# Performance work log

Measured on AMD Instinct MI355X. Metric: run time of the kernel, lower is better.

The kernel has to match this reference:

```python
import jax, jax.numpy as jnp
import numpy as np
from functools import partial

B, S, D, L, O, V = 32, 1024, 256, 4, 64, 5  # batch, seq, d_model, n_layers, output_dim, vocab
EPS = 1e-5
RC_MAP = jnp.array([3, 2, 1, 0, 4], dtype=jnp.int32)  # A<->T, C<->G, N->N


def layernorm(x, g, b):
    m = jnp.mean(x, axis=-1, keepdims=True)
    v = jnp.mean((x - m) ** 2, axis=-1, keepdims=True)
    return (x - m) * jax.lax.rsqrt(v + EPS) * g + b


def gru(x, w_ih, w_hh, b_ih, b_hh):
    """torch nn.GRU (single layer, batch_first) equivalent.
    x: (B,S,D); w_ih: (3H,D); w_hh: (3H,H); gates ordered r,z,n."""
    H = w_hh.shape[1]
    # precompute input contributions for all timesteps: (S,B,3H)
    xi = (jnp.einsum('bsd,gd->bsg', x, w_ih) + b_ih).transpose(1, 0, 2)

    def step(h, xt):
        gh = h @ w_hh.T + b_hh                      # (B,3H)
        xr, xz, xn = jnp.split(xt, 3, axis=-1)
        hr, hz, hn = jnp.split(gh, 3, axis=-1)
        r = jax.nn.sigmoid(xr + hr)
        z = jax.nn.sigmoid(xz + hz)
        n = jnp.tanh(xn + r * hn)
        h2 = (1.0 - z) * n + z * h
        return h2, h2

    h0 = jnp.zeros((x.shape[0], H), dtype=x.dtype)
    _, out = jax.lax.scan(step, h0, xi)
    return out.transpose(1, 0, 2)                   # (B,S,H)


def setup_inputs() -> dict:
    key = jax.random.key(0)
    ks = jax.random.split(key, 32)
    n = lambda k, shp, s=0.02: (jax.random.normal(k, shp, dtype=jnp.float32) * s)
    inp = {
        'tokens': jax.random.randint(ks[0], (B, S), 0, V),
        'emb':    n(ks[1], (V, D), 1.0),
        'pos':    n(ks[2], (1, S, D)),
        # per-layer stacked params (leading dim L)
        'ln_g':   jnp.ones((L, D), jnp.float32),
        'ln_b':   jnp.zeros((L, D), jnp.float32),
        'wih_f':  n(ks[3], (L, 3 * D, D)),
        'whh_f':  n(ks[4], (L, 3 * D, D)),
        'bih_f':  n(ks[5], (L, 3 * D)),
        'bhh_f':  n(ks[6], (L, 3 * D)),
        'wih_r':  n(ks[7], (L, 3 * D, D)),
        'whh_r':  n(ks[8], (L, 3 * D, D)),
        'bih_r':  n(ks[9], (L, 3 * D)),
        'bhh_r':  n(ks[10], (L, 3 * D)),
        'wg':     n(ks[11], (L, D, 2 * D)),
        'bg':     n(ks[12], (L, D)),
        'wo':     n(ks[13], (L, D, D)),
        'bo':     n(ks[14], (L, D)),
        'fn_g':   jnp.ones((D,), jnp.float32),
        'fn_b':   jnp.zeros((D,), jnp.float32),
        'pw':     n(ks[15], (O, D)),
        'pb':     n(ks[16], (O,)),
        'pln_g':  jnp.ones((O,), jnp.float32),
        'pln_b':  jnp.zeros((O,), jnp.float32),
    }
    return inp


def reference(tokens, emb, pos, ln_g, ln_b,
              wih_f, whh_f, bih_f, bhh_f,
              wih_r, whh_r, bih_r, bhh_r,
              wg, bg, wo, bo, fn_g, fn_b, pw, pb, pln_g, pln_b):
    def encode(tok):
        h = emb[tok] + pos[:, :tok.shape[1], :]      # (B,S,D)
        for i in range(L):
            hn = layernorm(h, ln_g[i], ln_b[i])
            f = gru(hn, wih_f[i], whh_f[i], bih_f[i], bhh_f[i])
            r = jnp.flip(gru(jnp.flip(hn, 1), wih_r[i], whh_r[i], bih_r[i], bhh_r[i]), 1)
            g = jax.nn.sigmoid(jnp.concatenate([f, r], -1) @ wg[i].T + bg[i])
            c = g * f + (1.0 - g) * r
            h = c @ wo[i].T + bo[i] + h              # residual
        return layernorm(h, fn_g, fn_b)

    h = encode(tokens)
    rc_tokens = jnp.flip(RC_MAP[tokens], -1)         # reverse-complement
    h_rc = encode(rc_tokens)
    pooled = (h.mean(1) + h_rc.mean(1)) * 0.5        # (B,D)
    p = layernorm(pooled @ pw.T + pb, pln_g, pln_b)
    return jax.nn.gelu(p, approximate=False)         # (B,O)
```

## Files before the change

kernel.cpp:

```cpp
#include <hip/hip_runtime.h>
#include <stdint.h>

#define DEV __device__ __forceinline__

typedef unsigned short u16;
typedef __attribute__((ext_vector_type(8))) __bf16 bf16x8;
typedef __attribute__((ext_vector_type(4))) float f32x4;

DEV float bf2f(u16 u) {
    unsigned v = ((unsigned)u) << 16;
    float f;
    __builtin_memcpy(&f, &v, 4);
    return f;
}
DEV u16 f2bf(float x) {
    unsigned u;
    __builtin_memcpy(&u, &x, 4);
    return (u16)((u + 0x7FFFu + ((u >> 16) & 1u)) >> 16);
}
DEV float sigf(float x) {
    float e = __builtin_amdgcn_exp2f(-1.442695040888963f * x);
    return __builtin_amdgcn_rcpf(1.0f + e);
}
DEV f32x4 mfma16(bf16x8 a, bf16x8 b, f32x4 c) {
    return __builtin_amdgcn_mfma_f32_16x16x32_bf16(a, b, c, 0, 0, 0);
}

static constexpr size_t XROW = 1536;
static constexpr size_t XE = 32768 * XROW;
static constexpr float NL2E = -1.442695040888963f;
static constexpr float P2L2E = 2.885390081777927f;

__global__ void convert_w(const float* __restrict__ src, u16* __restrict__ dst,
                          int n_per, int stride_l, int total) {
    int idx = blockIdx.x * 256 + threadIdx.x;
    if (idx >= total) return;
    int l = idx / n_per;
    int r = idx - l * n_per;
    dst[(size_t)l * stride_l + r] = f2bf(src[idx]);
}

__global__ void convert_whh(const float* __restrict__ src, u16* __restrict__ dst, int dir_ofs) {
    int idx = blockIdx.x * 256 + threadIdx.x;
    int l = idx / 196608;
    int r = idx - l * 196608;
    float S = ((r >> 16) < 2) ? NL2E : P2L2E;
    dst[(size_t)l * 393216 + dir_ofs + r] = f2bf(src[idx] * S);
}

__global__ void convert_wih(const float* __restrict__ src, const float* __restrict__ lng,
                            u16* __restrict__ dst, int dir_ofs) {
    int idx = blockIdx.x * 256 + threadIdx.x;
    int l = idx / 196608;
    int r = idx - l * 196608;
    int k = idx & 255;
    float S = ((r >> 16) < 2) ? NL2E : P2L2E;
    dst[(size_t)l * 393216 + dir_ofs + r] = f2bf(src[idx] * lng[l * 256 + k] * S);
}

__global__ void head_vecs_kernel(const float* __restrict__ wihf, const float* __restrict__ wihr,
                                 const float* __restrict__ bihf, const float* __restrict__ bihr,
                                 const float* __restrict__ bhhf, const float* __restrict__ bhhr,
                                 const float* __restrict__ lng, const float* __restrict__ lnb,
                                 float* __restrict__ env, float* __restrict__ cvec) {
    int w = threadIdx.x >> 6, lane = threadIdx.x & 63;
    int row = blockIdx.x * 4 + w;
    int l = row / 1536;
    int n1536 = row - l * 1536;
    int dir = n1536 >= 768;
    int n = n1536 - dir * 768;
    const float* W = (dir ? wihr : wihf) + ((size_t)l * 768 + n) * 256 + lane * 4;
    float4 wv = *(const float4*)W;
    float4 gv = *(const float4*)(lng + l * 256 + lane * 4);
    float4 bv = *(const float4*)(lnb + l * 256 + lane * 4);
    float es = wv.x * gv.x + wv.y * gv.y + wv.z * gv.z + wv.w * gv.w;
    float cs = wv.x * bv.x + wv.y * bv.y + wv.z * bv.z + wv.w * bv.w;
#pragma unroll
    for (int off = 1; off < 64; off <<= 1) {
        es += __shfl_xor(es, off);
        cs += __shfl_xor(cs, off);
    }
    if (lane == 0) {
        float S = (n < 512) ? NL2E : P2L2E;
        float c = cs + (dir ? bihr : bihf)[l * 768 + n];
        if (n < 512) c += (dir ? bhhr : bhhf)[l * 768 + n];
        env[row] = es * S;
        cvec[row] = c * S;
    }
}

__global__ void embed_kernel(const int* __restrict__ tok, const float* __restrict__ emb,
                             const float* __restrict__ pos, u16* __restrict__ h) {
    int row = blockIdx.x;
    int k = threadIdx.x;
    int e = row >> 15;
    int rem = row & 32767;
    int b = rem >> 10;
    int s = rem & 1023;
    int t0 = (e == 0) ? tok[b * 1024 + s] : tok[b * 1024 + (1023 - s)];
    if (e == 1) t0 = (t0 < 4) ? (3 - t0) : 4;
    h[(size_t)row * 256 + k] = f2bf(emb[t0 * 256 + k] + pos[s * 256 + k]);
}

__global__ void ln_stats_kernel(const u16* __restrict__ h, float2* __restrict__ stats) {
    int w = threadIdx.x >> 6, lane = threadIdx.x & 63;
    int row = blockIdx.x * 4 + w;
    int e = row >> 15;
    int rem = row & 32767;
    int b = rem >> 10;
    int s = rem & 1023;
    ushort4 v = *(const ushort4*)(h + (size_t)row * 256 + lane * 4);
    float x0 = bf2f(v.x), x1 = bf2f(v.y), x2 = bf2f(v.z), x3 = bf2f(v.w);
    float sum = x0 + x1 + x2 + x3;
    float sq = x0 * x0 + x1 * x1 + x2 * x2 + x3 * x3;
#pragma unroll
    for (int off = 1; off < 64; off <<= 1) {
        sum += __shfl_xor(sum, off);
        sq += __shfl_xor(sq, off);
    }
    if (lane == 0) {
        float mean = sum * (1.0f / 256.0f);
        float var = sq * (1.0f / 256.0f) - mean * mean;
        stats[e * 32768 + s * 32 + b] = make_float2(mean, rsqrtf(var + 1e-5f));
    }
}

template <int OP>
__global__ __launch_bounds__(256, 2) void gemm_bt(
    const u16* __restrict__ hin, const u16* __restrict__ Bw,
    const float* __restrict__ bias0, const float* __restrict__ bias1,
    u16* xibuf, const float2* __restrict__ stats, u16* hres) {
    constexpr int KK = (OP == 1) ? 512 : 256;
    constexpr int NKB = KK / 64;
    __shared__ __align__(16) u16 As[2][128 * 64];
    __shared__ __align__(16) u16 Bs[2][128 * 64];
    const int tid = threadIdx.x;
    const int lane = tid & 63, w = tid >> 6;
    const int l15 = lane & 15, q = lane >> 4;
    const int l8 = lane & 7, r8 = lane >> 3;
    const int e = blockIdx.z;
    const int m0 = blockIdx.x * 128, n0 = blockIdx.y * 128;
    const int wm = w & 1, wn = w >> 1;

    uint4 ra[4], rb[4];
    auto loadS = [&](int kb) {
#pragma unroll
        for (int i = 0; i < 4; ++i) {
            int row = w * 32 + i * 8 + r8;
            int c = l8 ^ (row & 7);
            int mrow = m0 + row;
            const u16* ap;
            if constexpr (OP == 0) {
                int bb = mrow & 31, ss = mrow >> 5;
                ap = hin + ((size_t)e * 32768 + bb * 1024 + ss) * 256 + kb * 64;
            } else if constexpr (OP == 1) {
                int colbase = (kb >= 4) ? 768 : 0;
                ap = xibuf + (size_t)e * XE + (size_t)mrow * XROW + colbase + (kb & 3) * 64;
            } else {
                ap = xibuf + (size_t)e * XE + (size_t)mrow * XROW + 256 + kb * 64;
            }
            ra[i] = *(const uint4*)(ap + c * 8);
            rb[i] = *(const uint4*)(Bw + (size_t)(n0 + row) * KK + kb * 64 + c * 8);
        }
    };
    auto writeS = [&](int buf) {
#pragma unroll
        for (int i = 0; i < 4; ++i) {
            int row = w * 32 + i * 8 + r8;
            *(uint4*)&As[buf][row * 64 + l8 * 8] = ra[i];
            *(uint4*)&Bs[buf][row * 64 + l8 * 8] = rb[i];
        }
    };

    f32x4 acc[4][4];
#pragma unroll
    for (int i = 0; i < 4; ++i)
#pragma unroll
        for (int j = 0; j < 4; ++j) acc[i][j] = (f32x4){0.f, 0.f, 0.f, 0.f};

    loadS(0);
    writeS(0);
    for (int kb = 0; kb < NKB; ++kb) {
        if (kb + 1 < NKB) loadS(kb + 1);
        __syncthreads();
        const int buf = kb & 1;
#pragma unroll
        for (int kt = 0; kt < 2; ++kt) {
            bf16x8 af[4], bfr[4];
#pragma unroll
            for (int i = 0; i < 4; ++i) {
                int rowa = wm * 64 + i * 16 + l15;
                int rowb = wn * 64 + i * 16 + l15;
                int c = kt * 4 + q;
                af[i] = *(const bf16x8*)&As[buf][rowa * 64 + (c ^ (rowa & 7)) * 8];
                bfr[i] = *(const bf16x8*)&Bs[buf][rowb * 64 + (c ^ (rowb & 7)) * 8];
            }
#pragma unroll
            for (int i = 0; i < 4; ++i)
#pragma unroll
                for (int j = 0; j < 4; ++j) acc[i][j] = mfma16(af[i], bfr[j], acc[i][j]);
        }
        if (kb + 1 < NKB) writeS((kb + 1) & 1);
    }

#pragma unroll
    for (int i = 0; i < 4; ++i) {
        const int mb = m0 + wm * 64 + i * 16 + q * 4;
        float2 st[4];
        if constexpr (OP == 0) {
#pragma unroll
            for (int r = 0; r < 4; ++r) st[r] = stats[e * 32768 + mb + r];
        }
#pragma unroll
        for (int jt = 0; jt < 4; ++jt) {
            const int nn = n0 + wn * 64 + jt * 16 + l15;
            f32x4 a = acc[i][jt];
            if constexpr (OP == 0) {
                const float en = bias0[nn], cn = bias1[nn];
#pragma unroll
                for (int r = 0; r < 4; ++r) {
                    float val = a[r] * st[r].y - st[r].x * st[r].y * en + cn;
                    xibuf[(size_t)e * XE + (size_t)(mb + r) * XROW + nn] = f2bf(val);
                }
            } else if constexpr (OP == 1) {
                const float bs = bias0[nn];
#pragma unroll
                for (int r = 0; r < 4; ++r) {
                    u16* xr_ = xibuf + (size_t)e * XE + (size_t)(mb + r) * XROW;
                    float gg = sigf(a[r] + bs);
                    float fv = bf2f(xr_[nn]), rv = bf2f(xr_[768 + nn]);
                    xr_[256 + nn] = f2bf(gg * fv + (1.0f - gg) * rv);
                }
            } else {
                const float bs = bias0[nn];
#pragma unroll
                for (int r = 0; r < 4; ++r) {
                    const int mm = mb + r;
                    size_t idx = ((size_t)e * 32768 + (size_t)(mm & 31) * 1024 + (mm >> 5)) * 256 + nn;
                    hres[idx] = f2bf(bf2f(hres[idx]) + a[r] + bs);
                }
            }
        }
    }
}

__global__ __launch_bounds__(512, 2) void scan_kernel(
    u16* xi, const u16* __restrict__ whh,
    const float* __restrict__ bhhf, const float* __restrict__ bhhr) {
    __shared__ __align__(16) u16 h_lds[16 * 264];
    const int tid = threadIdx.x;
    const int w = tid >> 6, lane = tid & 63;
    const int l15 = lane & 15, q = lane >> 4;
    const int bid = blockIdx.x;
    const int bh = bid & 1, d = (bid >> 1) & 1, e = bid >> 2;
    const int jb = w * 32;

    const u16* W = whh + (size_t)d * 196608;
    bf16x8 wf[3][2][8];
#pragma unroll
    for (int g = 0; g < 3; ++g)
#pragma unroll
        for (int jc = 0; jc < 2; ++jc)
#pragma unroll
            for (int kt = 0; kt < 8; ++kt)
                wf[g][jc][kt] = *(const bf16x8*)(
                    W + (size_t)(g * 256 + jb + jc * 16 + l15) * 256 + kt * 32 + q * 8);

    const float* bnp = (d ? bhhr : bhhf) + 512;
    f32x4 bn[2];
#pragma unroll
    for (int jc = 0; jc < 2; ++jc)
#pragma unroll
        for (int r = 0; r < 4; ++r) bn[jc][r] = P2L2E * bnp[jb + jc * 16 + q * 4 + r];

    const int s0 = d ? 1023 : 0;
    const ptrdiff_t step = (d ? -32 : 32) * (ptrdiff_t)XROW;
    u16* p = xi + (size_t)e * XE + (size_t)(s0 * 32 + bh * 16 + l15) * XROW + d * 768 + jb + q * 4;

    const int lrow = l15 * 264;
    const int jcol = jb + q * 4;

    ushort4 xvv[3][2];
#pragma unroll
    for (int g = 0; g < 3; ++g)
#pragma unroll
        for (int jc = 0; jc < 2; ++jc)
            xvv[g][jc] = *(const ushort4*)(p + g * 256 + jc * 16);

    for (int t = 0; t < 1024; ++t) {
        f32x4 a0[2], a1[2], a2[2];
#pragma unroll
        for (int jc = 0; jc < 2; ++jc) {
            a0[jc] = (f32x4){0.f, 0.f, 0.f, 0.f};
            a1[jc] = (f32x4){0.f, 0.f, 0.f, 0.f};
            a2[jc] = bn[jc];
        }
        if (t > 0) {
#pragma unroll
            for (int kt = 0; kt < 8; ++kt) {
                bf16x8 hb = *(const bf16x8*)&h_lds[lrow + kt * 32 + q * 8];
#pragma unroll
                for (int jc = 0; jc < 2; ++jc) {
                    a0[jc] = mfma16(wf[0][jc][kt], hb, a0[jc]);
                    a1[jc] = mfma16(wf[1][jc][kt], hb, a1[jc]);
                    a2[jc] = mfma16(wf[2][jc][kt], hb, a2[jc]);
                }
            }
        }
        ushort4 hs[2];
#pragma unroll
        for (int jc = 0; jc < 2; ++jc) {
            ushort4 hp4 = (t > 0) ? *(const ushort4*)&h_lds[lrow + jcol + jc * 16]
                                  : (ushort4){0, 0, 0, 0};
            u16 hr[4];
#pragma unroll
            for (int r = 0; r < 4; ++r) {
                float xr = bf2f(((const u16*)&xvv[0][jc])[r]);
                float xz = bf2f(((const u16*)&xvv[1][jc])[r]);
                float xn = bf2f(((const u16*)&xvv[2][jc])[r]);
                float rg = __builtin_amdgcn_rcpf(1.0f + __builtin_amdgcn_exp2f(xr + a0[jc][r]));
                float zg = __builtin_amdgcn_rcpf(1.0f + __builtin_amdgcn_exp2f(xz + a1[jc][r]));
                float E = __builtin_amdgcn_exp2f(__builtin_fmaf(rg, a2[jc][r], xn));
                float ng = (E - 1.0f) * __builtin_amdgcn_rcpf(E + 1.0f);
                float hp = (t > 0) ? bf2f(((const u16*)&hp4)[r]) : 0.f;
                float h2 = __builtin_fmaf(zg, hp - ng, ng);
                hr[r] = f2bf(h2);
            }
            hs[jc] = (ushort4){hr[0], hr[1], hr[2], hr[3]};
        }
        *(ushort4*)(p + 0) = hs[0];
        *(ushort4*)(p + 16) = hs[1];
        __syncthreads();
        *(ushort4*)&h_lds[lrow + jcol] = hs[0];
        *(ushort4*)&h_lds[lrow + jcol + 16] = hs[1];
        __syncthreads();
        if (t + 1 < 1024) {
            p += step;
#pragma unroll
            for (int g = 0; g < 3; ++g)
#pragma unroll
                for (int jc = 0; jc < 2; ++jc)
                    xvv[g][jc] = *(const ushort4*)(p + g * 256 + jc * 16);
        }
    }
}

__global__ __launch_bounds__(256) void pool_head_kernel(
    const u16* __restrict__ h, const float* __restrict__ fng, const float* __restrict__ fnb,
    const float* __restrict__ pw, const float* __restrict__ pb,
    const float* __restrict__ plng, const float* __restrict__ plnb, float* __restrict__ out) {
    __shared__ float pacc[4][256];
    __shared__ float pooled[256];
    const int b = blockIdx.x;
    const int tid = threadIdx.x;
    const int w = tid >> 6, lane = tid & 63;
    float a0 = 0.f, a1 = 0.f, a2 = 0.f, a3 = 0.f;
    for (int rr = w; rr < 2048; rr += 4) {
        int e = rr >> 10, s = rr & 1023;
        const u16* src = h + ((size_t)e * 32768 + (size_t)b * 1024 + s) * 256 + lane * 4;
        ushort4 v = *(const ushort4*)src;
        float x0 = bf2f(v.x), x1 = bf2f(v.y), x2 = bf2f(v.z), x3 = bf2f(v.w);
        float sum = x0 + x1 + x2 + x3;
        float sq = x0 * x0 + x1 * x1 + x2 * x2 + x3 * x3;
#pragma unroll
        for (int off = 1; off < 64; off <<= 1) {
            sum += __shfl_xor(sum, off);
            sq += __shfl_xor(sq, off);
        }
        float mean = sum * (1.0f / 256.0f);
        float var = sq * (1.0f / 256.0f) - mean * mean;
        float rs = rsqrtf(var + 1e-5f);
        a0 += (x0 - mean) * rs;
        a1 += (x1 - mean) * rs;
        a2 += (x2 - mean) * rs;
        a3 += (x3 - mean) * rs;
    }
    pacc[w][lane * 4 + 0] = a0;
    pacc[w][lane * 4 + 1] = a1;
    pacc[w][lane * 4 + 2] = a2;
    pacc[w][lane * 4 + 3] = a3;
    __syncthreads();
    {
        int k = tid;
        float t = pacc[0][k] + pacc[1][k] + pacc[2][k] + pacc[3][k];
        pooled[k] = (t * fng[k] + 2048.0f * fnb[k]) * (0.5f / 1024.0f);
    }
    __syncthreads();
    if (tid < 64) {
        float p = pb[tid];
        const float* wrow = pw + tid * 256;
        for (int k = 0; k < 256; ++k) p += pooled[k] * wrow[k];
        float sum = p;
#pragma unroll
        for (int off = 1; off < 64; off <<= 1) sum += __shfl_xor(sum, off);
        float mean = sum * (1.0f / 64.0f);
        float dv = p - mean;
        float sq = dv * dv;
#pragma unroll
        for (int off = 1; off < 64; off <<= 1) sq += __shfl_xor(sq, off);
        float var = sq * (1.0f / 64.0f);
        float y = dv * rsqrtf(var + 1e-5f) * plng[tid] + plnb[tid];
        out[b * 64 + tid] = y * 0.5f * (1.0f + erff(y * 0.70710678118654752f));
    }
}

extern "C" void kernel_launch(void* const* d_in, const int* in_sizes, int n_in,
                              void* d_out, int out_size, void* d_ws, size_t ws_size,
                              hipStream_t stream) {
    (void)in_sizes; (void)n_in; (void)out_size; (void)ws_size;
    const int* tokens = (const int*)d_in[0];
    const float* emb = (const float*)d_in[1];
    const float* pos = (const float*)d_in[2];
    const float* ln_g = (const float*)d_in[3];
    const float* ln_b = (const float*)d_in[4];
    const float* wih_f = (const float*)d_in[5];
    const float* whh_f = (const float*)d_in[6];
    const float* bih_f = (const float*)d_in[7];
    const float* bhh_f = (const float*)d_in[8];
    const float* wih_r = (const float*)d_in[9];
    const float* whh_r = (const float*)d_in[10];
    const float* bih_r = (const float*)d_in[11];
    const float* bhh_r = (const float*)d_in[12];
    const float* wg = (const float*)d_in[13];
    const float* bg = (const float*)d_in[14];
    const float* wo = (const float*)d_in[15];
    const float* bo = (const float*)d_in[16];
    const float* fn_g = (const float*)d_in[17];
    const float* fn_b = (const float*)d_in[18];
    const float* pw = (const float*)d_in[19];
    const float* pb = (const float*)d_in[20];
    const float* pln_g = (const float*)d_in[21];
    const float* pln_b = (const float*)d_in[22];
    float* out = (float*)d_out;
    char* ws = (char*)d_ws;

    u16* h = (u16*)(ws + 0);
    u16* xi = (u16*)(ws + 33554432);
    u16* wih_cat = (u16*)(ws + 234881024);
    u16* whh_bf = (u16*)(ws + 238026752);
    u16* wg_bf = (u16*)(ws + 241172480);
    u16* wo_bf = (u16*)(ws + 242221056);
    float* env = (float*)(ws + 242745344);
    float* cvec = (float*)(ws + 242769920);
    float2* stats = (float2*)(ws + 242794496);

    convert_wih<<<3072, 256, 0, stream>>>(wih_f, ln_g, wih_cat, 0);
    convert_wih<<<3072, 256, 0, stream>>>(wih_r, ln_g, wih_cat, 196608);
    convert_whh<<<3072, 256, 0, stream>>>(whh_f, whh_bf, 0);
    convert_whh<<<3072, 256, 0, stream>>>(whh_r, whh_bf, 196608);
    convert_w<<<2048, 256, 0, stream>>>(wg, wg_bf, 131072, 131072, 524288);
    convert_w<<<1024, 256, 0, stream>>>(wo, wo_bf, 65536, 65536, 262144);
    head_vecs_kernel<<<1536, 256, 0, stream>>>(wih_f, wih_r, bih_f, bih_r, bhh_f, bhh_r,
                                               ln_g, ln_b, env, cvec);
    embed_kernel<<<65536, 256, 0, stream>>>(tokens, emb, pos, h);

    for (int i = 0; i < 4; ++i) {
        ln_stats_kernel<<<16384, 256, 0, stream>>>(h, stats);
        gemm_bt<0><<<dim3(256, 12, 2), 256, 0, stream>>>(
            h, wih_cat + (size_t)i * 393216, env + i * 1536, cvec + i * 1536,
            xi, stats, nullptr);
        scan_kernel<<<8, 512, 0, stream>>>(
            xi, whh_bf + (size_t)i * 393216, bhh_f + i * 768, bhh_r + i * 768);
        gemm_bt<1><<<dim3(256, 2, 2), 256, 0, stream>>>(
            nullptr, wg_bf + (size_t)i * 131072, bg + i * 256, nullptr,
            xi, nullptr, nullptr);
        gemm_bt<2><<<dim3(256, 2, 2), 256, 0, stream>>>(
            nullptr, wo_bf + (size_t)i * 65536, bo + i * 256, nullptr,
            xi, nullptr, h);
    }
    pool_head_kernel<<<32, 256, 0, stream>>>(h, fn_g, fn_b, pw, pb, pln_g, pln_b, out);
}
```

Before: 10.37 ms.

## Fuse LayerNorm stats into input-projection GEMM with resident A tile

Removes the separate ln_stats kernel and computes per-row mean and rstd inside a new gemm_xi kernel while loading the full 128x256 activation tile into LDS. Each block keeps its A tile resident and loops over all 12 N tiles of the 1536-wide weight, register-prefetching the next B tile. This cuts a kernel launch, the stats round trip through global memory, and the repeated A reloads across N-tile blocks. The cost is a 128KB LDS footprint at one block per CU and only 512 blocks, so there is less parallelism and latency hiding.

```diff
diff --git a/kernel.cpp b/kernel.cpp
--- a/kernel.cpp
+++ b/kernel.cpp
@@ -102,34 +102,146 @@
     h[(size_t)row * 256 + k] = f2bf(emb[t0 * 256 + k] + pos[s * 256 + k]);
 }
 
-__global__ void ln_stats_kernel(const u16* __restrict__ h, float2* __restrict__ stats) {
-    int w = threadIdx.x >> 6, lane = threadIdx.x & 63;
-    int row = blockIdx.x * 4 + w;
-    int e = row >> 15;
-    int rem = row & 32767;
-    int b = rem >> 10;
-    int s = rem & 1023;
-    ushort4 v = *(const ushort4*)(h + (size_t)row * 256 + lane * 4);
-    float x0 = bf2f(v.x), x1 = bf2f(v.y), x2 = bf2f(v.z), x3 = bf2f(v.w);
-    float sum = x0 + x1 + x2 + x3;
-    float sq = x0 * x0 + x1 * x1 + x2 * x2 + x3 * x3;
-#pragma unroll
-    for (int off = 1; off < 64; off <<= 1) {
-        sum += __shfl_xor(sum, off);
-        sq += __shfl_xor(sq, off);
-    }
-    if (lane == 0) {
-        float mean = sum * (1.0f / 256.0f);
-        float var = sq * (1.0f / 256.0f) - mean * mean;
-        stats[e * 32768 + s * 32 + b] = make_float2(mean, rsqrtf(var + 1e-5f));
+__global__ __launch_bounds__(256, 1) void gemm_xi(
+    const u16* __restrict__ hin, const u16* __restrict__ Bw,
+    const float* __restrict__ env, const float* __restrict__ cvec,
+    u16* __restrict__ xibuf) {
+    __shared__ __align__(16) u16 Ah[128 * 256];
+    __shared__ __align__(16) u16 Bsh[128 * 256];
+    __shared__ float2 stats_s[128];
+    const int tid = threadIdx.x;
+    const int lane = tid & 63, w = tid >> 6;
+    const int l15 = lane & 15, q = lane >> 4;
+    const int l8 = lane & 7, r8 = lane >> 3;
+    const int e = blockIdx.z;
+    const int m0 = blockIdx.x * 128;
+    const int wm = w & 1, wn = w >> 1;
+
+    float sm0 = 0.f, sm1 = 0.f, sm2 = 0.f, sm3 = 0.f;
+    float sq0 = 0.f, sq1 = 0.f, sq2 = 0.f, sq3 = 0.f;
+#pragma unroll
+    for (int i = 0; i < 4; ++i) {
+        const int row = w * 32 + i * 8 + r8;
+        const int mrow = m0 + row;
+        const int bb = mrow & 31, ss = mrow >> 5;
+        const u16* ap = hin + ((size_t)e * 32768 + bb * 1024 + ss) * 256;
+        const int c = l8 ^ (row & 7);
+        float s = 0.f, s2 = 0.f;
+#pragma unroll
+        for (int kb = 0; kb < 4; ++kb) {
+            uint4 v = *(const uint4*)(ap + kb * 64 + c * 8);
+            *(uint4*)&Ah[row * 256 + kb * 64 + l8 * 8] = v;
+            const u16* pv = (const u16*)&v;
+#pragma unroll
+            for (int x = 0; x < 8; ++x) {
+                float f = bf2f(pv[x]);
+                s += f;
+                s2 += f * f;
+            }
+        }
+        if (i == 0) { sm0 = s; sq0 = s2; }
+        if (i == 1) { sm1 = s; sq1 = s2; }
+        if (i == 2) { sm2 = s; sq2 = s2; }
+        if (i == 3) { sm3 = s; sq3 = s2; }
+    }
+#pragma unroll
+    for (int off = 1; off < 8; off <<= 1) {
+        sm0 += __shfl_xor(sm0, off); sq0 += __shfl_xor(sq0, off);
+        sm1 += __shfl_xor(sm1, off); sq1 += __shfl_xor(sq1, off);
+        sm2 += __shfl_xor(sm2, off); sq2 += __shfl_xor(sq2, off);
+        sm3 += __shfl_xor(sm3, off); sq3 += __shfl_xor(sq3, off);
+    }
+    if (l8 == 0) {
+#pragma unroll
+        for (int i = 0; i < 4; ++i) {
+            float s = (i == 0) ? sm0 : (i == 1) ? sm1 : (i == 2) ? sm2 : sm3;
+            float s2 = (i == 0) ? sq0 : (i == 1) ? sq1 : (i == 2) ? sq2 : sq3;
+            float mean = s * (1.0f / 256.0f);
+            float var = s2 * (1.0f / 256.0f) - mean * mean;
+            stats_s[w * 32 + i * 8 + r8] = make_float2(mean, rsqrtf(var + 1e-5f));
+        }
+    }
+
+    uint4 rbv[16];
+    auto loadB = [&](int nt) {
+#pragma unroll
+        for (int i = 0; i < 4; ++i) {
+            const int row = w * 32 + i * 8 + r8;
+            const int c = l8 ^ (row & 7);
+            const u16* bp = Bw + (size_t)(nt * 128 + row) * 256;
+#pragma unroll
+            for (int kb = 0; kb < 4; ++kb)
+                rbv[kb * 4 + i] = *(const uint4*)(bp + kb * 64 + c * 8);
+        }
+    };
+    auto writeB = [&]() {
+#pragma unroll
+        for (int i = 0; i < 4; ++i) {
+            const int row = w * 32 + i * 8 + r8;
+#pragma unroll
+            for (int kb = 0; kb < 4; ++kb)
+                *(uint4*)&Bsh[row * 256 + kb * 64 + l8 * 8] = rbv[kb * 4 + i];
+        }
+    };
+    loadB(0);
+    writeB();
+    __syncthreads();
+
+    for (int nt = 0; nt < 12; ++nt) {
+        if (nt + 1 < 12) loadB(nt + 1);
+        f32x4 acc[4][4];
+#pragma unroll
+        for (int i = 0; i < 4; ++i)
+#pragma unroll
+            for (int j = 0; j < 4; ++j) acc[i][j] = (f32x4){0.f, 0.f, 0.f, 0.f};
+#pragma unroll
+        for (int ks = 0; ks < 8; ++ks) {
+            const int K8 = ks * 4 + q;
+            const int kb = K8 >> 3, c = K8 & 7;
+            bf16x8 af[4], bfr[4];
+#pragma unroll
+            for (int i = 0; i < 4; ++i) {
+                int rowa = wm * 64 + i * 16 + l15;
+                int rowb = wn * 64 + i * 16 + l15;
+                af[i] = *(const bf16x8*)&Ah[rowa * 256 + kb * 64 + ((c ^ (rowa & 7)) * 8)];
+                bfr[i] = *(const bf16x8*)&Bsh[rowb * 256 + kb * 64 + ((c ^ (rowb & 7)) * 8)];
+            }
+#pragma unroll
+            for (int i = 0; i < 4; ++i)
+#pragma unroll
+                for (int j = 0; j < 4; ++j) acc[i][j] = mfma16(af[i], bfr[j], acc[i][j]);
+        }
+#pragma unroll
+        for (int i = 0; i < 4; ++i) {
+            const int ml = wm * 64 + i * 16 + q * 4;
+            const int mb = m0 + ml;
+            float2 st[4];
+#pragma unroll
+            for (int r = 0; r < 4; ++r) st[r] = stats_s[ml + r];
+#pragma unroll
+            for (int jt = 0; jt < 4; ++jt) {
+                const int nn = nt * 128 + wn * 64 + jt * 16 + l15;
+                f32x4 a = acc[i][jt];
+                const float en = env[nn], cn = cvec[nn];
+#pragma unroll
+                for (int r = 0; r < 4; ++r) {
+                    float val = a[r] * st[r].y - st[r].x * st[r].y * en + cn;
+                    xibuf[(size_t)e * XE + (size_t)(mb + r) * XROW + nn] = f2bf(val);
+                }
+            }
+        }
+        if (nt + 1 < 12) {
+            __syncthreads();
+            writeB();
+            __syncthreads();
+        }
     }
 }
 
 template <int OP>
 __global__ __launch_bounds__(256, 2) void gemm_bt(
-    const u16* __restrict__ hin, const u16* __restrict__ Bw,
-    const float* __restrict__ bias0, const float* __restrict__ bias1,
-    u16* xibuf, const float2* __restrict__ stats, u16* hres) {
+    const u16* __restrict__ Bw, const float* __restrict__ bias0,
+    u16* xibuf, u16* hres) {
     constexpr int KK = (OP == 1) ? 512 : 256;
     constexpr int NKB = KK / 64;
     __shared__ __align__(16) u16 As[2][128 * 64];
@@ -150,10 +262,7 @@
             int c = l8 ^ (row & 7);
             int mrow = m0 + row;
             const u16* ap;
-            if constexpr (OP == 0) {
-                int bb = mrow & 31, ss = mrow >> 5;
-                ap = hin + ((size_t)e * 32768 + bb * 1024 + ss) * 256 + kb * 64;
-            } else if constexpr (OP == 1) {
+            if constexpr (OP == 1) {
                 int colbase = (kb >= 4) ? 768 : 0;
                 ap = xibuf + (size_t)e * XE + (size_t)mrow * XROW + colbase + (kb & 3) * 64;
             } else {
@@ -206,24 +315,12 @@
 #pragma unroll
     for (int i = 0; i < 4; ++i) {
         const int mb = m0 + wm * 64 + i * 16 + q * 4;
-        float2 st[4];
-        if constexpr (OP == 0) {
-#pragma unroll
-            for (int r = 0; r < 4; ++r) st[r] = stats[e * 32768 + mb + r];
-        }
 #pragma unroll
         for (int jt = 0; jt < 4; ++jt) {
             const int nn = n0 + wn * 64 + jt * 16 + l15;
             f32x4 a = acc[i][jt];
-            if constexpr (OP == 0) {
-                const float en = bias0[nn], cn = bias1[nn];
-#pragma unroll
-                for (int r = 0; r < 4; ++r) {
-                    float val = a[r] * st[r].y - st[r].x * st[r].y * en + cn;
-                    xibuf[(size_t)e * XE + (size_t)(mb + r) * XROW + nn] = f2bf(val);
-                }
-            } else if constexpr (OP == 1) {
-                const float bs = bias0[nn];
+            const float bs = bias0[nn];
+            if constexpr (OP == 1) {
 #pragma unroll
                 for (int r = 0; r < 4; ++r) {
                     u16* xr_ = xibuf + (size_t)e * XE + (size_t)(mb + r) * XROW;
@@ -232,7 +329,6 @@
                     xr_[256 + nn] = f2bf(gg * fv + (1.0f - gg) * rv);
                 }
             } else {
-                const float bs = bias0[nn];
 #pragma unroll
                 for (int r = 0; r < 4; ++r) {
                     const int mm = mb + r;
@@ -442,7 +538,6 @@
     u16* wo_bf = (u16*)(ws + 242221056);
     float* env = (float*)(ws + 242745344);
     float* cvec = (float*)(ws + 242769920);
-    float2* stats = (float2*)(ws + 242794496);
 
     convert_wih<<<3072, 256, 0, stream>>>(wih_f, ln_g, wih_cat, 0);
     convert_wih<<<3072, 256, 0, stream>>>(wih_r, ln_g, wih_cat, 196608);
@@ -455,18 +550,14 @@
     embed_kernel<<<65536, 256, 0, stream>>>(tokens, emb, pos, h);
 
     for (int i = 0; i < 4; ++i) {
-        ln_stats_kernel<<<16384, 256, 0, stream>>>(h, stats);
-        gemm_bt<0><<<dim3(256, 12, 2), 256, 0, stream>>>(
-            h, wih_cat + (size_t)i * 393216, env + i * 1536, cvec + i * 1536,
-            xi, stats, nullptr);
+        gemm_xi<<<dim3(256, 1, 2), 256, 0, stream>>>(
+            h, wih_cat + (size_t)i * 393216, env + i * 1536, cvec + i * 1536, xi);
         scan_kernel<<<8, 512, 0, stream>>>(
             xi, whh_bf + (size_t)i * 393216, bhh_f + i * 768, bhh_r + i * 768);
         gemm_bt<1><<<dim3(256, 2, 2), 256, 0, stream>>>(
-            nullptr, wg_bf + (size_t)i * 131072, bg + i * 256, nullptr,
-            xi, nullptr, nullptr);
+            wg_bf + (size_t)i * 131072, bg + i * 256, xi, nullptr);
         gemm_bt<2><<<dim3(256, 2, 2), 256, 0, stream>>>(
-            nullptr, wo_bf + (size_t)i * 65536, bo + i * 256, nullptr,
-            xi, nullptr, h);
+            wo_bf + (size_t)i * 65536, bo + i * 256, xi, h);
     }
     pool_head_kernel<<<32, 256, 0, stream>>>(h, fn_g, fn_b, pw, pb, pln_g, pln_b, out);
 }
```

Result: no change. 10.50 ms (+1.2%).
